# Kernel optimization log

Measured on AMD Instinct MI355X. Metric: run time of the kernel, lower is better.

Reference implementation:

```python
import jax, jax.numpy as jnp
import numpy as np
import math

LAMB = 0.2
N_ITERS = 3
HALF_PLUS_HALF_LOG2PI = 0.5 + 0.5 * math.log(2.0 * math.pi)  # 1/2 + log(2*pi)/2
SQRT_2PI = math.sqrt(2.0 * math.pi)


def _safe_div(num, den):
    # tf.math.divide_no_nan: 0 where denominator is 0
    den_ok = jnp.where(den == 0, 1.0, den)
    return jnp.where(den == 0, 0.0, num / den_ok)


def _m_step(act_in, R, V, bias_a, bias_b):
    # act_in: [B,ci], R: [B or 1,ci,co], V: [B,ci,co,q,s]
    odds = act_in[:, :, None] * R                                        # [B,ci,co]
    r = _safe_div(odds, jnp.sum(odds, axis=1, keepdims=True))[:, :, :, None, None]
    mu = jnp.sum(r * V, axis=1, keepdims=True)                           # [B,1,co,q,s]
    sigma = jnp.sqrt(jnp.sum(r * (V - mu) ** 2, axis=1, keepdims=True))  # [B,1,co,q,s]
    cost = jnp.sum(r * jnp.log(sigma) + HALF_PLUS_HALF_LOG2PI, axis=1)   # [B,co,q,s]
    logits = LAMB * (bias_a
                     - bias_b * jnp.sum(r, axis=(1, 3, 4))
                     - jnp.sum(cost, axis=(2, 3)))                       # [B,co]
    act_out = jax.nn.softmax(logits, axis=-1)
    return act_out, jnp.sum(mu, axis=1), sigma                           # mu -> [B,co,q,s]


def _e_step(act_out, V, mu, sigma):
    # Normal(mu, sigma).prob(V); mu broadcast over capsules_in axis
    d = V - mu[:, None]                                                  # [B,ci,co,q,s]
    prob = jnp.exp(-0.5 * d * d / (sigma * sigma)) / (sigma * SQRT_2PI)
    raw_R = act_out[:, None, :, None, None] * prob                       # [B,ci,co,q,s]
    # tf.linalg.norm(ord=1, axis=None) = global sum of |raw_R| over the whole tensor
    normed = _safe_div(raw_R, jnp.sum(jnp.abs(raw_R)))
    return jnp.sum(normed, axis=(3, 4))                                  # [B,ci,co]


def setup_inputs() -> dict:
    key = jax.random.key(0)
    k1, k2, k3, k4, k5 = jax.random.split(key, 5)
    B, CI, CO, P, S = 16, 512, 128, 8, 8
    act = jax.random.uniform(k1, (B, CI), dtype=jnp.float32)
    pose = jax.random.normal(k2, (B, CI, P, P), dtype=jnp.float32)
    transitions = 0.05 * jax.random.normal(k3, (CI, CO, P, S), dtype=jnp.float32)
    bias_a = 0.05 * jax.random.normal(k4, (CO,), dtype=jnp.float32)
    bias_b = 0.05 * jax.random.normal(k5, (CO,), dtype=jnp.float32)
    return {"act": act, "pose": pose, "transitions": transitions,
            "bias_a": bias_a, "bias_b": bias_b}


def reference(act, pose, transitions, bias_a, bias_b):
    CI = act.shape[1]
    CO = transitions.shape[1]
    posed = jnp.swapaxes(pose, -1, -2)                 # transPOSE=True
    # votes: pose[:, :, None, :, :] @ transitions  -> [B,ci,co,q,s]
    V = jnp.einsum('biqp,iops->bioqs', posed, transitions)
    R = jnp.full((1, CI, CO), 1.0 / CO, dtype=V.dtype)
    act_out, mu, sigma = _m_step(act, R, V, bias_a, bias_b)
    for _ in range(N_ITERS - 1):
        R = _e_step(act_out, V, mu, sigma)
        act_out, mu, sigma = _m_step(act, R, V, bias_a, bias_b)
    return act_out, mu
```

## Files before the change

### kernel.cpp

```cpp
#include <hip/hip_runtime.h>
#include <hip/hip_bf16.h>

#define B_    16
#define CI_   512
#define CO_   128
#define QS    64
#define NWAVE 16
#define IPW   (CI_ / NWAVE)

static constexpr float LAMB = 0.2f;
static constexpr float NEG_HALF_LOG2E = -0.72134752044448170368f;

template <int CTRL>
__device__ __forceinline__ float dpp_add(float v) {
    int x = __builtin_bit_cast(int, v);
    int y = __builtin_amdgcn_update_dpp(x, x, CTRL, 0xF, 0xF, false);
    return v + __builtin_bit_cast(float, y);
}

__device__ __forceinline__ float wave_sum64_shfl(float v) {
#pragma unroll
    for (int m = 32; m >= 1; m >>= 1) v += __shfl_xor(v, m, 64);
    return v;
}

__global__ __launch_bounds__(256) void transpose_kernel(
    const float* __restrict__ pose, const float* __restrict__ trans,
    float* __restrict__ poseT, float* __restrict__ TT)
{
    const int bid    = blockIdx.x;
    const bool isPose = bid >= 4096;
    const float* __restrict__ src = isPose ? pose  : trans;
    float*       __restrict__ dst = isPose ? poseT : TT;
    const int base4 = (isPose ? bid - 4096 : bid) * 256 + threadIdx.x;
    const int u     = base4 & 15;
    const int m0    = ((base4 >> 4) << 6) + ((u & 1) << 5) + (u >> 1);
    float4 v;
    v.x = src[m0];
    v.y = src[m0 + 8];
    v.z = src[m0 + 16];
    v.w = src[m0 + 24];
    ((float4*)dst)[base4] = v;
}

__global__
__attribute__((amdgpu_flat_work_group_size(1024, 1024), amdgpu_waves_per_eu(4, 8)))
void capsule_kernel(
    const float* __restrict__ poseT,
    const float* __restrict__ TT,
    const float* __restrict__ act,
    const float* __restrict__ bias_a,
    const float* __restrict__ bias_b,
    float* __restrict__ logits,
    float* __restrict__ mu_out)
{
    const int blk = blockIdx.x;
    const int xcd = blk & 7;
    const int idx = blk >> 3;
    const int o   = xcd + ((idx & 15) << 3);
    const int b   = idx >> 4;

    const int tid  = threadIdx.x;
    const int wave = tid >> 6;
    const int lane = tid & 63;
    const int q    = lane >> 3;
    const int s    = lane & 7;
    const int i0   = wave * IPW;

    const float4* pT4  = (const float4*)poseT + ((size_t)(b * CI_ + i0)) * 16 + q * 2;
    const float4* tT4  = (const float4*)TT    + ((size_t)(i0 * CO_ + o)) * 16 + s * 2;
    const float*  actb = act + b * CI_ + i0;

    __shared__ __align__(16) float prbuf[NWAVE][8 * 68];
    __shared__ __align__(16) float wbuf[NWAVE * 32];
    __shared__ __align__(16) float2 sAB [NWAVE][QS];
    __shared__ __align__(16) float2 sAB2[4][QS];
    __shared__ float sC [NWAVE];
    __shared__ float sC2[4];

    float* prw = prbuf[wave];

    float V[IPW];
    float Sw = 0.f, SwV = 0.f, SwV2 = 0.f;

#pragma unroll
    for (int j = 0; j < IPW; ++j) {
        float4 a0 = pT4[j * 16];
        float4 a1 = pT4[j * 16 + 1];
        float4 b0 = tT4[(size_t)j * (CO_ * 16)];
        float4 b1 = tT4[(size_t)j * (CO_ * 16) + 1];
        float v;
        v = a0.x * b0.x;
        v = fmaf(a0.y, b0.y, v);
        v = fmaf(a0.z, b0.z, v);
        v = fmaf(a0.w, b0.w, v);
        v = fmaf(a1.x, b1.x, v);
        v = fmaf(a1.y, b1.y, v);
        v = fmaf(a1.z, b1.z, v);
        v = fmaf(a1.w, b1.w, v);
        V[j] = v;
        float ai = actb[j];
        Sw  += ai;
        SwV  = fmaf(ai, v, SwV);
        SwV2 = fmaf(ai * v, v, SwV2);
    }

    auto block_reduce = [&]() {
        sAB[wave][lane] = make_float2(SwV, SwV2);
        if (lane == 0) sC[wave] = Sw;
        __syncthreads();
        if (wave < 4) {
            float2 t0 = sAB[wave * 4 + 0][lane];
            float2 t1 = sAB[wave * 4 + 1][lane];
            float2 t2 = sAB[wave * 4 + 2][lane];
            float2 t3 = sAB[wave * 4 + 3][lane];
            float2 r;
            r.x = (t0.x + t1.x) + (t2.x + t3.x);
            r.y = (t0.y + t1.y) + (t2.y + t3.y);
            sAB2[wave][lane] = r;
            if (lane == 0)
                sC2[wave] = (sC[wave * 4 + 0] + sC[wave * 4 + 1]) +
                            (sC[wave * 4 + 2] + sC[wave * 4 + 3]);
        }
        __syncthreads();
        float2 u0 = sAB2[0][lane];
        float2 u1 = sAB2[1][lane];
        float2 u2 = sAB2[2][lane];
        float2 u3 = sAB2[3][lane];
        SwV  = (u0.x + u1.x) + (u2.x + u3.x);
        SwV2 = (u0.y + u1.y) + (u2.y + u3.y);
        Sw   = (sC2[0] + sC2[1]) + (sC2[2] + sC2[3]);
    };

    block_reduce();
    float invSw = (Sw != 0.f) ? 1.f / Sw : 0.f;
    float mu  = SwV * invSw;
    float var = fmaxf(fmaf(-mu, mu, SwV2 * invSw), 1e-30f);
    float is  = 1.f / sqrtf(var);

#pragma unroll 1
    for (int it = 0; it < 2; ++it) {
        const float cc = is * is * NEG_HALF_LOG2E;
#pragma unroll
        for (int p = 0; p < 4; ++p) {
#pragma unroll
            for (int jj = 0; jj < 8; ++jj) {
                float d = V[p * 8 + jj] - mu;
                prw[jj * 68 + lane] = exp2f(d * cc * d);
            }
            const int r  = lane >> 3;
            const int co = (lane & 7) * 8;
            const float4* rp = (const float4*)&prw[r * 68 + co];
            float4 x0 = rp[0], x1 = rp[1];
            float ps = ((x0.x + x0.y) + (x0.z + x0.w)) +
                       ((x1.x + x1.y) + (x1.z + x1.w));
            ps = dpp_add<0xB1>(ps);
            ps = dpp_add<0x4E>(ps);
            ps = dpp_add<0x141>(ps);
            float wj = actb[p * 8 + r] * ps;
            if ((lane & 7) == 0) wbuf[wave * 32 + p * 8 + r] = wj;
        }
        const float4* wb4 = (const float4*)&wbuf[wave * 32];
        Sw = 0.f; SwV = 0.f; SwV2 = 0.f;
#pragma unroll
        for (int k = 0; k < 8; ++k) {
            float4 w4 = wb4[k];
            float v0 = V[4 * k + 0], v1 = V[4 * k + 1];
            float v2 = V[4 * k + 2], v3 = V[4 * k + 3];
            Sw += w4.x; SwV = fmaf(w4.x, v0, SwV); SwV2 = fmaf(w4.x * v0, v0, SwV2);
            Sw += w4.y; SwV = fmaf(w4.y, v1, SwV); SwV2 = fmaf(w4.y * v1, v1, SwV2);
            Sw += w4.z; SwV = fmaf(w4.z, v2, SwV); SwV2 = fmaf(w4.z * v2, v2, SwV2);
            Sw += w4.w; SwV = fmaf(w4.w, v3, SwV); SwV2 = fmaf(w4.w * v3, v3, SwV2);
        }
        block_reduce();
        invSw = (Sw != 0.f) ? 1.f / Sw : 0.f;
        mu  = SwV * invSw;
        var = fmaxf(fmaf(-mu, mu, SwV2 * invSw), 1e-30f);
        is  = 1.f / sqrtf(var);
    }

    if (wave == 0) {
        mu_out[((size_t)b * CO_ + o) * QS + lane] = mu;
        float sl = wave_sum64_shfl(0.5f * logf(var));
        if (lane == 0)
            logits[b * CO_ + o] = LAMB * (bias_a[o] - bias_b[o] - sl);
    }
}

__global__ __launch_bounds__(256, 4) void capsule_legacy(
    const float* __restrict__ pose,
    const float* __restrict__ trans,
    const float* __restrict__ act,
    const float* __restrict__ bias_a,
    const float* __restrict__ bias_b,
    float* __restrict__ logits,
    float* __restrict__ mu_out)
{
    const int blk  = blockIdx.x;
    const int b    = blk >> 7;
    const int o    = blk & 127;
    const int tid  = threadIdx.x;
    const int wave = tid >> 6;
    const int lane = tid & 63;
    const int q    = lane >> 3;
    const int s    = lane & 7;
    const int i0   = wave * 128;

    const float* poseb = pose + ((size_t)b * CI_ + i0) * QS + lane;
    const float* tb    = trans + ((size_t)i0 * CO_ + o) * QS + lane;
    const float* actb  = act + b * CI_ + i0;

    __shared__ float sSwV[4][QS];
    __shared__ float sSwV2[4][QS];
    __shared__ float sSw[4];

    float Sw = 0.f, SwV = 0.f, SwV2 = 0.f;

    auto do_sweep = [&](bool use_prob, float mu_r, float is_r) {
        Sw = 0.f; SwV = 0.f; SwV2 = 0.f;
        for (int j = 0; j < 128; ++j) {
            float pe = poseb[(size_t)j * QS];
            float te = tb[(size_t)j * (CO_ * QS)];
            float ai = actb[j];
            float V = 0.f;
#pragma unroll
            for (int p = 0; p < 8; ++p) {
                float a = __shfl(pe, p * 8 + q, 64);
                float t = __shfl(te, p * 8 + s, 64);
                V = fmaf(a, t, V);
            }
            float w;
            if (use_prob) {
                float d  = V - mu_r;
                float e  = d * is_r;
                float pr = is_r * exp2f(e * e * NEG_HALF_LOG2E);
                w = ai * wave_sum64_shfl(pr);
            } else {
                w = ai;
            }
            Sw += w;
            SwV  = fmaf(w, V, SwV);
            SwV2 = fmaf(w * V, V, SwV2);
        }
        __syncthreads();
        sSwV[wave][lane]  = SwV;
        sSwV2[wave][lane] = SwV2;
        if (lane == 0) sSw[wave] = Sw;
        __syncthreads();
        float a = 0.f, c = 0.f, d2 = 0.f;
#pragma unroll
        for (int w2 = 0; w2 < 4; ++w2) {
            a  += sSwV[w2][lane];
            d2 += sSwV2[w2][lane];
            c  += sSw[w2];
        }
        SwV = a; SwV2 = d2; Sw = c;
    };

    float mu = 0.f, var = 1.f, is = 1.f;
    do_sweep(false, 0.f, 0.f);
    {
        float invSw = (Sw != 0.f) ? 1.f / Sw : 0.f;
        mu = SwV * invSw; var = fmaxf(fmaf(-mu, mu, SwV2 * invSw), 1e-30f);
        is = 1.f / sqrtf(var);
    }
    do_sweep(true, mu, is);
    {
        float invSw = (Sw != 0.f) ? 1.f / Sw : 0.f;
        mu = SwV * invSw; var = fmaxf(fmaf(-mu, mu, SwV2 * invSw), 1e-30f);
        is = 1.f / sqrtf(var);
    }
    do_sweep(true, mu, is);
    {
        float invSw = (Sw != 0.f) ? 1.f / Sw : 0.f;
        mu = SwV * invSw; var = fmaxf(fmaf(-mu, mu, SwV2 * invSw), 1e-30f);
    }

    if (wave == 0) {
        mu_out[((size_t)b * CO_ + o) * QS + lane] = mu;
        float sl = wave_sum64_shfl(0.5f * logf(var));
        if (lane == 0)
            logits[b * CO_ + o] = LAMB * (bias_a[o] - bias_b[o] - sl);
    }
}

__global__ __launch_bounds__(128) void softmax_kernel(
    const float* __restrict__ logits, float* __restrict__ out)
{
    const int b = blockIdx.x;
    const int t = threadIdx.x;
    float l = logits[b * CO_ + t];

    __shared__ float sm[2];
    __shared__ float s2[2];

    float m = l;
#pragma unroll
    for (int k = 32; k >= 1; k >>= 1) m = fmaxf(m, __shfl_xor(m, k, 64));
    if ((t & 63) == 0) sm[t >> 6] = m;
    __syncthreads();
    m = fmaxf(sm[0], sm[1]);

    float e = expf(l - m);
    float ssum = e;
#pragma unroll
    for (int k = 32; k >= 1; k >>= 1) ssum += __shfl_xor(ssum, k, 64);
    if ((t & 63) == 0) s2[t >> 6] = ssum;
    __syncthreads();
    float tot = s2[0] + s2[1];

    out[b * CO_ + t] = e / tot;
}

extern "C" void kernel_launch(void* const* d_in, const int* in_sizes, int n_in,
                              void* d_out, int out_size, void* d_ws, size_t ws_size,
                              hipStream_t stream) {
    const float *act = nullptr, *pose = nullptr, *trans = nullptr;
    const float *bias_a = nullptr, *bias_b = nullptr;
    for (int i = 0; i < n_in; ++i) {
        const float* p = (const float*)d_in[i];
        switch (in_sizes[i]) {
            case 8192:    act = p; break;
            case 524288:  pose = p; break;
            case 4194304: trans = p; break;
            case 128:     if (!bias_a) bias_a = p; else bias_b = p; break;
            default: break;
        }
    }
    if (!act || !pose || !trans || !bias_a || !bias_b) {
        act    = (const float*)d_in[0];
        pose   = (const float*)d_in[1];
        trans  = (const float*)d_in[2];
        bias_a = (const float*)d_in[3];
        bias_b = (const float*)d_in[4];
    }

    float* out_act = (float*)d_out;
    float* out_mu  = out_act + B_ * CO_;

    const size_t NEEDED = (size_t)(524288 + 4194304 + 2048) * 4;

    if (ws_size >= NEEDED) {
        float* poseT  = (float*)d_ws;
        float* TT     = poseT + 524288;
        float* logits = TT + 4194304;

        transpose_kernel<<<dim3(4608), dim3(256), 0, stream>>>(
            pose, trans, poseT, TT);
        capsule_kernel<<<dim3(B_ * CO_), dim3(1024), 0, stream>>>(
            poseT, TT, act, bias_a, bias_b, logits, out_mu);
        softmax_kernel<<<dim3(B_), dim3(128), 0, stream>>>(logits, out_act);
    } else {
        float* logits = (float*)d_ws;
        capsule_legacy<<<dim3(B_ * CO_), dim3(256), 0, stream>>>(
            pose, trans, act, bias_a, bias_b, logits, out_mu);
        softmax_kernel<<<dim3(B_), dim3(128), 0, stream>>>(logits, out_act);
    }
}
```

Before: 274.5 us.

## Process eight batches per block to cut grid to 256 blocks

Each block now loops over eight batch elements for a single output capsule, so the launch shrinks from 2048 to 256 blocks of 1024 threads. The XCD-to-output mapping is changed so each XCD handles 16 contiguous outputs, which is meant to improve L2 reuse of the transition matrix slices across batches. The per-batch work inside a block runs serially with a scheduling barrier between iterations. This risks lower occupancy and less latency hiding: 256 blocks of 1024 threads may not cover all CUs with multiple blocks, and the transition loads are reissued for every batch rather than held in registers.

Result: slower. 675.6 us (+146.1%).

```diff
diff --git a/kernel.cpp b/kernel.cpp
--- a/kernel.cpp
+++ b/kernel.cpp
@@ -54,11 +54,11 @@
     float* __restrict__ logits,
     float* __restrict__ mu_out)
 {
-    const int blk = blockIdx.x;
-    const int xcd = blk & 7;
-    const int idx = blk >> 3;
-    const int o   = xcd + ((idx & 15) << 3);
-    const int b   = idx >> 4;
+    const int bi  = blockIdx.x;
+    const int xcd = bi & 7;
+    const int y   = bi >> 3;
+    const int o   = xcd * 16 + (y & 15);
+    const int b0  = (y >> 4) * 8;
 
     const int tid  = threadIdx.x;
     const int wave = tid >> 6;
@@ -67,9 +67,7 @@
     const int s    = lane & 7;
     const int i0   = wave * IPW;
 
-    const float4* pT4  = (const float4*)poseT + ((size_t)(b * CI_ + i0)) * 16 + q * 2;
-    const float4* tT4  = (const float4*)TT    + ((size_t)(i0 * CO_ + o)) * 16 + s * 2;
-    const float*  actb = act + b * CI_ + i0;
+    const float4* tT4 = (const float4*)TT + ((size_t)(i0 * CO_ + o)) * 16 + s * 2;
 
     __shared__ __align__(16) float prbuf[NWAVE][8 * 68];
     __shared__ __align__(16) float wbuf[NWAVE * 32];
@@ -80,110 +78,118 @@
 
     float* prw = prbuf[wave];
 
-    float V[IPW];
-    float Sw = 0.f, SwV = 0.f, SwV2 = 0.f;
-
-#pragma unroll
-    for (int j = 0; j < IPW; ++j) {
-        float4 a0 = pT4[j * 16];
-        float4 a1 = pT4[j * 16 + 1];
-        float4 b0 = tT4[(size_t)j * (CO_ * 16)];
-        float4 b1 = tT4[(size_t)j * (CO_ * 16) + 1];
-        float v;
-        v = a0.x * b0.x;
-        v = fmaf(a0.y, b0.y, v);
-        v = fmaf(a0.z, b0.z, v);
-        v = fmaf(a0.w, b0.w, v);
-        v = fmaf(a1.x, b1.x, v);
-        v = fmaf(a1.y, b1.y, v);
-        v = fmaf(a1.z, b1.z, v);
-        v = fmaf(a1.w, b1.w, v);
-        V[j] = v;
-        float ai = actb[j];
-        Sw  += ai;
-        SwV  = fmaf(ai, v, SwV);
-        SwV2 = fmaf(ai * v, v, SwV2);
-    }
-
-    auto block_reduce = [&]() {
-        sAB[wave][lane] = make_float2(SwV, SwV2);
-        if (lane == 0) sC[wave] = Sw;
-        __syncthreads();
-        if (wave < 4) {
-            float2 t0 = sAB[wave * 4 + 0][lane];
-            float2 t1 = sAB[wave * 4 + 1][lane];
-            float2 t2 = sAB[wave * 4 + 2][lane];
-            float2 t3 = sAB[wave * 4 + 3][lane];
-            float2 r;
-            r.x = (t0.x + t1.x) + (t2.x + t3.x);
-            r.y = (t0.y + t1.y) + (t2.y + t3.y);
-            sAB2[wave][lane] = r;
+#pragma unroll 1
+    for (int pair = 0; pair < 8; ++pair) {
+        const int b = b0 + pair;
+        const float4* pT4  = (const float4*)poseT + ((size_t)(b * CI_ + i0)) * 16 + q * 2;
+        const float*  actb = act + b * CI_ + i0;
+
+        float V[IPW];
+        float Sw = 0.f, SwV = 0.f, SwV2 = 0.f;
+
+#pragma unroll
+        for (int j = 0; j < IPW; ++j) {
+            float4 a0 = pT4[j * 16];
+            float4 a1 = pT4[j * 16 + 1];
+            float4 b0v = tT4[(size_t)j * (CO_ * 16)];
+            float4 b1v = tT4[(size_t)j * (CO_ * 16) + 1];
+            float v;
+            v = a0.x * b0v.x;
+            v = fmaf(a0.y, b0v.y, v);
+            v = fmaf(a0.z, b0v.z, v);
+            v = fmaf(a0.w, b0v.w, v);
+            v = fmaf(a1.x, b1v.x, v);
+            v = fmaf(a1.y, b1v.y, v);
+            v = fmaf(a1.z, b1v.z, v);
+            v = fmaf(a1.w, b1v.w, v);
+            V[j] = v;
+            float ai = actb[j];
+            Sw  += ai;
+            SwV  = fmaf(ai, v, SwV);
+            SwV2 = fmaf(ai * v, v, SwV2);
+        }
+
+        auto block_reduce = [&]() {
+            sAB[wave][lane] = make_float2(SwV, SwV2);
+            if (lane == 0) sC[wave] = Sw;
+            __syncthreads();
+            if (wave < 4) {
+                float2 t0 = sAB[wave * 4 + 0][lane];
+                float2 t1 = sAB[wave * 4 + 1][lane];
+                float2 t2 = sAB[wave * 4 + 2][lane];
+                float2 t3 = sAB[wave * 4 + 3][lane];
+                float2 r;
+                r.x = (t0.x + t1.x) + (t2.x + t3.x);
+                r.y = (t0.y + t1.y) + (t2.y + t3.y);
+                sAB2[wave][lane] = r;
+                if (lane == 0)
+                    sC2[wave] = (sC[wave * 4 + 0] + sC[wave * 4 + 1]) +
+                                (sC[wave * 4 + 2] + sC[wave * 4 + 3]);
+            }
+            __syncthreads();
+            float2 u0 = sAB2[0][lane];
+            float2 u1 = sAB2[1][lane];
+            float2 u2 = sAB2[2][lane];
+            float2 u3 = sAB2[3][lane];
+            SwV  = (u0.x + u1.x) + (u2.x + u3.x);
+            SwV2 = (u0.y + u1.y) + (u2.y + u3.y);
+            Sw   = (sC2[0] + sC2[1]) + (sC2[2] + sC2[3]);
+        };
+
+        block_reduce();
+        float invSw = (Sw != 0.f) ? 1.f / Sw : 0.f;
+        float mu  = SwV * invSw;
+        float var = fmaxf(fmaf(-mu, mu, SwV2 * invSw), 1e-30f);
+        float is  = 1.f / sqrtf(var);
+
+#pragma unroll 1
+        for (int it = 0; it < 2; ++it) {
+            const float cc = is * is * NEG_HALF_LOG2E;
+#pragma unroll
+            for (int p = 0; p < 4; ++p) {
+#pragma unroll
+                for (int jj = 0; jj < 8; ++jj) {
+                    float d = V[p * 8 + jj] - mu;
+                    prw[jj * 68 + lane] = exp2f(d * cc * d);
+                }
+                const int r  = lane >> 3;
+                const int co = (lane & 7) * 8;
+                const float4* rp = (const float4*)&prw[r * 68 + co];
+                float4 x0 = rp[0], x1 = rp[1];
+                float ps = ((x0.x + x0.y) + (x0.z + x0.w)) +
+                           ((x1.x + x1.y) + (x1.z + x1.w));
+                ps = dpp_add<0xB1>(ps);
+                ps = dpp_add<0x4E>(ps);
+                ps = dpp_add<0x141>(ps);
+                float wj = actb[p * 8 + r] * ps;
+                if ((lane & 7) == 0) wbuf[wave * 32 + p * 8 + r] = wj;
+            }
+            const float4* wb4 = (const float4*)&wbuf[wave * 32];
+            Sw = 0.f; SwV = 0.f; SwV2 = 0.f;
+#pragma unroll
+            for (int k = 0; k < 8; ++k) {
+                float4 w4 = wb4[k];
+                float v0 = V[4 * k + 0], v1 = V[4 * k + 1];
+                float v2 = V[4 * k + 2], v3 = V[4 * k + 3];
+                Sw += w4.x; SwV = fmaf(w4.x, v0, SwV); SwV2 = fmaf(w4.x * v0, v0, SwV2);
+                Sw += w4.y; SwV = fmaf(w4.y, v1, SwV); SwV2 = fmaf(w4.y * v1, v1, SwV2);
+                Sw += w4.z; SwV = fmaf(w4.z, v2, SwV); SwV2 = fmaf(w4.z * v2, v2, SwV2);
+                Sw += w4.w; SwV = fmaf(w4.w, v3, SwV); SwV2 = fmaf(w4.w * v3, v3, SwV2);
+            }
+            block_reduce();
+            invSw = (Sw != 0.f) ? 1.f / Sw : 0.f;
+            mu  = SwV * invSw;
+            var = fmaxf(fmaf(-mu, mu, SwV2 * invSw), 1e-30f);
+            is  = 1.f / sqrtf(var);
+        }
+
+        if (wave == 0) {
+            mu_out[((size_t)b * CO_ + o) * QS + lane] = mu;
+            float sl = wave_sum64_shfl(0.5f * logf(var));
             if (lane == 0)
-                sC2[wave] = (sC[wave * 4 + 0] + sC[wave * 4 + 1]) +
-                            (sC[wave * 4 + 2] + sC[wave * 4 + 3]);
-        }
-        __syncthreads();
-        float2 u0 = sAB2[0][lane];
-        float2 u1 = sAB2[1][lane];
-        float2 u2 = sAB2[2][lane];
-        float2 u3 = sAB2[3][lane];
-        SwV  = (u0.x + u1.x) + (u2.x + u3.x);
-        SwV2 = (u0.y + u1.y) + (u2.y + u3.y);
-        Sw   = (sC2[0] + sC2[1]) + (sC2[2] + sC2[3]);
-    };
-
-    block_reduce();
-    float invSw = (Sw != 0.f) ? 1.f / Sw : 0.f;
-    float mu  = SwV * invSw;
-    float var = fmaxf(fmaf(-mu, mu, SwV2 * invSw), 1e-30f);
-    float is  = 1.f / sqrtf(var);
-
-#pragma unroll 1
-    for (int it = 0; it < 2; ++it) {
-        const float cc = is * is * NEG_HALF_LOG2E;
-#pragma unroll
-        for (int p = 0; p < 4; ++p) {
-#pragma unroll
-            for (int jj = 0; jj < 8; ++jj) {
-                float d = V[p * 8 + jj] - mu;
-                prw[jj * 68 + lane] = exp2f(d * cc * d);
-            }
-            const int r  = lane >> 3;
-            const int co = (lane & 7) * 8;
-            const float4* rp = (const float4*)&prw[r * 68 + co];
-            float4 x0 = rp[0], x1 = rp[1];
-            float ps = ((x0.x + x0.y) + (x0.z + x0.w)) +
-                       ((x1.x + x1.y) + (x1.z + x1.w));
-            ps = dpp_add<0xB1>(ps);
-            ps = dpp_add<0x4E>(ps);
-            ps = dpp_add<0x141>(ps);
-            float wj = actb[p * 8 + r] * ps;
-            if ((lane & 7) == 0) wbuf[wave * 32 + p * 8 + r] = wj;
-        }
-        const float4* wb4 = (const float4*)&wbuf[wave * 32];
-        Sw = 0.f; SwV = 0.f; SwV2 = 0.f;
-#pragma unroll
-        for (int k = 0; k < 8; ++k) {
-            float4 w4 = wb4[k];
-            float v0 = V[4 * k + 0], v1 = V[4 * k + 1];
-            float v2 = V[4 * k + 2], v3 = V[4 * k + 3];
-            Sw += w4.x; SwV = fmaf(w4.x, v0, SwV); SwV2 = fmaf(w4.x * v0, v0, SwV2);
-            Sw += w4.y; SwV = fmaf(w4.y, v1, SwV); SwV2 = fmaf(w4.y * v1, v1, SwV2);
-            Sw += w4.z; SwV = fmaf(w4.z, v2, SwV); SwV2 = fmaf(w4.z * v2, v2, SwV2);
-            Sw += w4.w; SwV = fmaf(w4.w, v3, SwV); SwV2 = fmaf(w4.w * v3, v3, SwV2);
-        }
-        block_reduce();
-        invSw = (Sw != 0.f) ? 1.f / Sw : 0.f;
-        mu  = SwV * invSw;
-        var = fmaxf(fmaf(-mu, mu, SwV2 * invSw), 1e-30f);
-        is  = 1.f / sqrtf(var);
-    }
-
-    if (wave == 0) {
-        mu_out[((size_t)b * CO_ + o) * QS + lane] = mu;
-        float sl = wave_sum64_shfl(0.5f * logf(var));
-        if (lane == 0)
-            logits[b * CO_ + o] = LAMB * (bias_a[o] - bias_b[o] - sl);
+                logits[b * CO_ + o] = LAMB * (bias_a[o] - bias_b[o] - sl);
+        }
+        __builtin_amdgcn_sched_barrier(0);
     }
 }
 
@@ -347,7 +353,7 @@
 
         transpose_kernel<<<dim3(4608), dim3(256), 0, stream>>>(
             pose, trans, poseT, TT);
-        capsule_kernel<<<dim3(B_ * CO_), dim3(1024), 0, stream>>>(
+        capsule_kernel<<<dim3(256), dim3(1024), 0, stream>>>(
             poseT, TT, act, bias_a, bias_b, logits, out_mu);
         softmax_kernel<<<dim3(B_), dim3(128), 0, stream>>>(logits, out_act);
     } else {
```
